# Performance work log

Hardware: AMD Instinct MI355X
Metric: run time of the kernel (lower is better)

## Reference

```python
import jax, jax.numpy as jnp
import numpy as np

B, S, D, H = 2, 2048, 1024, 16
DK = D // H

def setup_inputs() -> dict:
    key = jax.random.key(0)
    k1, k2, k3 = jax.random.split(key, 3)
    std = 2.0 / (D + 3 * D)
    x = jax.random.normal(k1, (B, S, D), dtype=jnp.float32)
    W_qkv = jax.random.normal(k2, (3 * D, D), dtype=jnp.float32) * std
    W_out = jax.random.normal(k3, (D, D), dtype=jnp.float32) * (2.0 / (2 * D))
    return {"x": x, "W_qkv": W_qkv, "W_out": W_out}

def reference(x, W_qkv, W_out):
    # fused QKV projection: [..., d_in] x [d_out, d_in] -> [..., d_out]
    proj = jnp.einsum('bsd,ed->bse', x, W_qkv)               # [B,S,3*H*DK]
    proj = proj.reshape(B, S, 3, H, DK)
    q = proj[:, :, 0].transpose(0, 2, 1, 3)                  # [B,H,S,DK]
    k = proj[:, :, 1].transpose(0, 2, 1, 3)
    v = proj[:, :, 2].transpose(0, 2, 1, 3)
    scores = jnp.einsum('bhnd,bhmd->bhnm', q, k) / jnp.sqrt(jnp.float32(DK))
    causal = jnp.tril(jnp.ones((S, S), dtype=bool))
    scores = jnp.where(causal, scores, -jnp.inf)
    attn = jax.nn.softmax(scores, axis=-1)
    out = jnp.einsum('bhnm,bhmd->bhnd', attn, v)             # [B,H,S,DK]
    out = out.transpose(0, 2, 1, 3).reshape(B, S, H * DK)
    return jnp.einsum('bsd,ed->bse', out, W_out)             # [B,S,D]
```

## Files before the change

kernel.cpp:

```cpp
#include <hip/hip_runtime.h>
#include <hip/hip_bf16.h>
#include <stdint.h>

typedef __attribute__((ext_vector_type(8))) __bf16 bf16x8;
typedef __attribute__((ext_vector_type(8))) short  short8;
typedef __attribute__((ext_vector_type(4))) float  f32x4;

#define MFMA16(a, b, c) __builtin_amdgcn_mfma_f32_16x16x32_bf16((a), (b), (c), 0, 0, 0)

__device__ __forceinline__ unsigned short f32_bf16(float f) {
  union { float f; unsigned u; } v; v.f = f;
  unsigned r = v.u + 0x7FFFu + ((v.u >> 16) & 1u);
  return (unsigned short)(r >> 16);
}

__device__ __forceinline__ void gload16(const unsigned short* g, unsigned short* l) {
  __builtin_amdgcn_global_load_lds(
      (const __attribute__((address_space(1))) unsigned int*)(g),
      (__attribute__((address_space(3))) unsigned int*)(l), 16, 0, 0);
}

__global__ void cvt3_kernel(const float* __restrict__ a, int na4,
                            const float* __restrict__ b, int nb4,
                            const float* __restrict__ c, int nc4,
                            unsigned short* __restrict__ oa,
                            unsigned short* __restrict__ ob,
                            unsigned short* __restrict__ oc) {
  int total = na4 + nb4 + nc4;
  for (int i = blockIdx.x * blockDim.x + threadIdx.x; i < total; i += gridDim.x * blockDim.x) {
    const float* src; unsigned short* dst; int j = i;
    if (j < na4) { src = a; dst = oa; }
    else if (j - na4 < nb4) { j -= na4; src = b; dst = ob; }
    else { j -= na4 + nb4; src = c; dst = oc; }
    float4 v = reinterpret_cast<const float4*>(src)[j];
    ushort4 o4;
    o4.x = f32_bf16(v.x); o4.y = f32_bf16(v.y);
    o4.z = f32_bf16(v.z); o4.w = f32_bf16(v.w);
    reinterpret_cast<ushort4*>(dst)[j] = o4;
  }
}

template <int MODE>
__global__ __launch_bounds__(256) void gemm_bt(const unsigned short* __restrict__ A,
                                               const unsigned short* __restrict__ Bm,
                                               void* __restrict__ Cout,
                                               int M, int N, int K) {
  __shared__ unsigned short As[128 * 32];
  __shared__ unsigned short Bs[128 * 32];
  __shared__ unsigned short Es[2 * 64 * 64];
  const int tid  = threadIdx.x;
  const int lane = tid & 63;
  const int wid  = tid >> 6;
  const int wr   = wid >> 1, wc = wid & 1;
  const int l16  = lane & 15, lh = lane >> 4;
  const int m0   = blockIdx.y * 128;
  const int n0   = blockIdx.x * 128;

  f32x4 acc[4][4];
#pragma unroll
  for (int mi = 0; mi < 4; ++mi)
#pragma unroll
    for (int ni = 0; ni < 4; ++ni) acc[mi][ni] = 0.f;

  const int c0 = tid, c1 = 256 + tid;
  const unsigned short* a0 = A + (size_t)(m0 + (c0 >> 2)) * K + (c0 & 3) * 8;
  const unsigned short* a1 = A + (size_t)(m0 + (c1 >> 2)) * K + (c1 & 3) * 8;
  const unsigned short* b0 = Bm + (size_t)(n0 + (c0 >> 2)) * K + (c0 & 3) * 8;
  const unsigned short* b1 = Bm + (size_t)(n0 + (c1 >> 2)) * K + (c1 & 3) * 8;
  const int d0 = wid * 64 * 8;
  const int d1 = (256 + wid * 64) * 8;

  for (int k0 = 0; k0 < K; k0 += 32) {
    __syncthreads();
    gload16(a0 + k0, As + d0);
    gload16(a1 + k0, As + d1);
    gload16(b0 + k0, Bs + d0);
    gload16(b1 + k0, Bs + d1);
    __syncthreads();
    bf16x8 af[4], bfr[4];
#pragma unroll
    for (int i = 0; i < 4; ++i) {
      af[i]  = *(const bf16x8*)(As + (wr * 64 + i * 16 + l16) * 32 + lh * 8);
      bfr[i] = *(const bf16x8*)(Bs + (wc * 64 + i * 16 + l16) * 32 + lh * 8);
    }
#pragma unroll
    for (int mi = 0; mi < 4; ++mi)
#pragma unroll
      for (int ni = 0; ni < 4; ++ni)
        acc[mi][ni] = MFMA16(af[mi], bfr[ni], acc[mi][ni]);
  }

  if (MODE == 0) {
    __syncthreads();
    unsigned short* Ep = (wid == 0) ? As : (wid == 1) ? Bs : Es + (wid - 2) * 4096;
    const int gn0 = n0 + wc * 64;
    const int cc  = gn0 >> 10;
    const int hh2 = (gn0 & 1023) >> 6;
    const int gm0 = m0 + wr * 64;
    const int bb2 = gm0 >> 11;
    const int ss0 = gm0 & 2047;
    const int bh2 = bb2 * 16 + hh2;
    unsigned short* qkv = (unsigned short*)Cout;

    if (cc < 2) {
      const float qsc = (cc == 0) ? 0.18033688f : 1.0f;
#pragma unroll
      for (int mi = 0; mi < 4; ++mi)
#pragma unroll
        for (int ni = 0; ni < 4; ++ni)
#pragma unroll
          for (int r = 0; r < 4; ++r) {
            int row = mi * 16 + lh * 4 + r;
            int col = (ni * 16 + l16) ^ (lh << 3);
            Ep[row * 64 + col] = f32_bf16(acc[mi][ni][r] * qsc);
          }
      unsigned short* qk = qkv + (((size_t)cc * 32 + bh2) * 2048 + ss0) * 64;
#pragma unroll
      for (int it = 0; it < 8; ++it) {
        int ci = it * 64 + lane;
        int row = ci >> 3, c = ci & 7;
        short8 vv = *(const short8*)(Ep + row * 64 + ((c ^ ((row >> 2) & 3)) * 8));
        *(short8*)(qk + (size_t)row * 64 + c * 8) = vv;
      }
    } else {
#pragma unroll
      for (int mi = 0; mi < 4; ++mi)
#pragma unroll
        for (int ni = 0; ni < 4; ++ni) {
          int dk = ni * 16 + l16;
          int ssl = mi * 16 + lh * 4;
          unsigned lo, hi;
          asm("v_cvt_pk_bf16_f32 %0, %1, %2" : "=v"(lo) : "v"(acc[mi][ni][0]), "v"(acc[mi][ni][1]));
          asm("v_cvt_pk_bf16_f32 %0, %1, %2" : "=v"(hi) : "v"(acc[mi][ni][2]), "v"(acc[mi][ni][3]));
          int off = dk * 64 + (ssl ^ ((dk & 7) << 3));
          *(uint2*)(Ep + off) = make_uint2(lo, hi);
        }
      unsigned short* vt = qkv + (size_t)8388608 + (size_t)bh2 * 64 * 2048 + ss0;
#pragma unroll
      for (int it = 0; it < 8; ++it) {
        int ci = it * 64 + lane;
        int dk = ci >> 3, c = ci & 7;
        short8 vv = *(const short8*)(Ep + dk * 64 + ((c ^ (dk & 7)) * 8));
        *(short8*)(vt + (size_t)dk * 2048 + c * 8) = vv;
      }
    }
  } else {
    float* C = (float*)Cout;
#pragma unroll
    for (int mi = 0; mi < 4; ++mi)
#pragma unroll
      for (int ni = 0; ni < 4; ++ni)
#pragma unroll
        for (int r = 0; r < 4; ++r) {
          int gm = m0 + wr * 64 + mi * 16 + lh * 4 + r;
          int gn = n0 + wc * 64 + ni * 16 + l16;
          C[(size_t)gm * N + gn] = acc[mi][ni][r];
        }
  }
}

__global__ __launch_bounds__(256) void attn_kernel(const unsigned short* __restrict__ Qg,
                                                   const unsigned short* __restrict__ Kg,
                                                   const unsigned short* __restrict__ Vtg,
                                                   unsigned short* __restrict__ Og) {
  __shared__ unsigned short Ks[2][64 * 64];
  __shared__ unsigned short Vs[2][64 * 64];
  __shared__ unsigned short Pl[4][16 * 64];

  const int tid  = threadIdx.x;
  const int lane = tid & 63;
  const int w    = tid >> 6;
  const int l16  = lane & 15, lh = lane >> 4;
  const int qt   = 31 - (blockIdx.x >> 5);
  const int bh   = blockIdx.x & 31;
  const int bb   = bh >> 4, hh = bh & 15;
  const int qb   = qt * 64;
  const int wqb  = qb + w * 16;

  const unsigned short* Qh = Qg + (size_t)bh * (2048 * 64);
  const unsigned short* Kh = Kg + (size_t)bh * (2048 * 64);
  const unsigned short* Vh = Vtg + (size_t)bh * (64 * 2048);

  bf16x8 qf[2];
#pragma unroll
  for (int h2 = 0; h2 < 2; ++h2)
    qf[h2] = *(const bf16x8*)(Qh + (size_t)(wqb + l16) * 64 + h2 * 32 + lh * 8);

  float mreg = 0.f;
  float ll   = 0.f;
  f32x4 o[4];
#pragma unroll
  for (int f = 0; f < 4; ++f) o[f] = 0.f;

  const int sA = tid, sB = tid + 256;
  const int rA = sA >> 3, hA = (sA & 7) ^ (rA & 7);
  const int rB = sB >> 3, hB = (sB & 7) ^ (rB & 7);
  const unsigned short* kSrcA = Kh + rA * 64 + hA * 8;
  const unsigned short* kSrcB = Kh + rB * 64 + hB * 8;
  const unsigned short* vSrcA = Vh + (size_t)rA * 2048 + hA * 8;
  const unsigned short* vSrcB = Vh + (size_t)rB * 2048 + hB * 8;
  const int ldsA = w * 64 * 8;
  const int ldsB = (256 + w * 64) * 8;

  const int sw = l16 & 7;
  const int ntiles = qt + 1;

  gload16(kSrcA, &Ks[0][ldsA]);
  gload16(kSrcB, &Ks[0][ldsB]);
  gload16(vSrcA, &Vs[0][ldsA]);
  gload16(vSrcB, &Vs[0][ldsB]);
  __syncthreads();

  for (int t = 0; t < ntiles; ++t) {
    const int kv0 = t * 64;
    const int cur = t & 1;
    if (t + 1 < ntiles) {
      const int nk = kv0 + 64;
      gload16(kSrcA + (size_t)nk * 64, &Ks[cur ^ 1][ldsA]);
      gload16(kSrcB + (size_t)nk * 64, &Ks[cur ^ 1][ldsB]);
      gload16(vSrcA + nk, &Vs[cur ^ 1][ldsA]);
      gload16(vSrcB + nk, &Vs[cur ^ 1][ldsB]);
    }

    if (kv0 <= wqb + 15) {
      const unsigned short* Kb = Ks[cur];
      const unsigned short* Vb = Vs[cur];

      f32x4 st[4];
#pragma unroll
      for (int tt = 0; tt < 4; ++tt) {
        const unsigned short* krow = Kb + (tt * 16 + l16) * 64;
        bf16x8 kf0 = *(const bf16x8*)(krow + ((lh ^ sw) * 8));
        bf16x8 kf1 = *(const bf16x8*)(krow + (((lh + 4) ^ sw) * 8));
        f32x4 a = {0.f, 0.f, 0.f, 0.f};
        a = MFMA16(kf0, qf[0], a);
        a = MFMA16(kf1, qf[1], a);
        st[tt] = a;
      }

      if (kv0 + 63 > wqb) {
        int qrow = wqb + l16;
#pragma unroll
        for (int tt = 0; tt < 4; ++tt) {
          int kvb = kv0 + tt * 16 + lh * 4;
#pragma unroll
          for (int r = 0; r < 4; ++r)
            if (kvb + r > qrow) st[tt][r] = -__builtin_inff();
        }
      }

      float pm = fmaxf(fmaxf(st[0][0], st[0][1]), fmaxf(st[0][2], st[0][3]));
#pragma unroll
      for (int tt = 1; tt < 4; ++tt)
        pm = fmaxf(pm, fmaxf(fmaxf(st[tt][0], st[tt][1]), fmaxf(st[tt][2], st[tt][3])));
      if (!__all(pm <= mreg + 8.f)) {
        float t0 = pm;
        t0 = fmaxf(t0, __shfl_xor(t0, 16));
        t0 = fmaxf(t0, __shfl_xor(t0, 32));
        float mn = fmaxf(mreg, t0);
        float er = exp2f(mreg - mn);
        mreg = mn;
        ll *= er;
#pragma unroll
        for (int r = 0; r < 4; ++r) {
          float e = __shfl(er, lh * 4 + r);
#pragma unroll
          for (int f = 0; f < 4; ++f) o[f][r] *= e;
        }
      }

      unsigned short* Pw = Pl[w];
      int rbase = l16 * 64;
      float ps = 0.f;
#pragma unroll
      for (int tt = 0; tt < 4; ++tt) {
        float p0 = exp2f(st[tt][0] - mreg);
        float p1 = exp2f(st[tt][1] - mreg);
        float p2 = exp2f(st[tt][2] - mreg);
        float p3 = exp2f(st[tt][3] - mreg);
        ps += (p0 + p1) + (p2 + p3);
        unsigned lo, hi;
        asm("v_cvt_pk_bf16_f32 %0, %1, %2" : "=v"(lo) : "v"(p0), "v"(p1));
        asm("v_cvt_pk_bf16_f32 %0, %1, %2" : "=v"(hi) : "v"(p2), "v"(p3));
        int c8 = tt * 2 + (lh >> 1);
        int off = rbase + ((c8 ^ sw) << 3) + (lh & 1) * 4;
        *(uint2*)(Pw + off) = make_uint2(lo, hi);
      }
      float rs = ps;
      rs += __shfl_xor(rs, 16);
      rs += __shfl_xor(rs, 32);
      ll += rs;

      bf16x8 pf0 = *(const bf16x8*)(Pw + rbase + ((lh ^ sw) * 8));
      bf16x8 pf1 = *(const bf16x8*)(Pw + rbase + (((lh + 4) ^ sw) * 8));
#pragma unroll
      for (int f = 0; f < 4; ++f) {
        const unsigned short* vrow = Vb + (f * 16 + l16) * 64;
        bf16x8 vf0 = *(const bf16x8*)(vrow + ((lh ^ sw) * 8));
        bf16x8 vf1 = *(const bf16x8*)(vrow + (((lh + 4) ^ sw) * 8));
        o[f] = MFMA16(pf0, vf0, o[f]);
        o[f] = MFMA16(pf1, vf1, o[f]);
      }
    }
    __syncthreads();
  }

  unsigned short* op = Og + (size_t)bb * 2048 * 1024 + (size_t)hh * 64;
#pragma unroll
  for (int r = 0; r < 4; ++r) {
    float linv = 1.f / __shfl(ll, lh * 4 + r);
    int row = wqb + lh * 4 + r;
#pragma unroll
    for (int f = 0; f < 4; ++f)
      op[(size_t)row * 1024 + f * 16 + l16] = f32_bf16(o[f][r] * linv);
  }
}

extern "C" void kernel_launch(void* const* d_in, const int* in_sizes, int n_in,
                              void* d_out, int out_size, void* d_ws, size_t ws_size,
                              hipStream_t stream) {
  const float* x    = (const float*)d_in[0];
  const float* Wqkv = (const float*)d_in[1];
  const float* Wout = (const float*)d_in[2];
  float* out = (float*)d_out;

  char* ws = (char*)d_ws;
  unsigned short* xb  = (unsigned short*)(ws);
  unsigned short* wqb = (unsigned short*)(ws + (size_t)8 * 1024 * 1024);
  unsigned short* wob = (unsigned short*)(ws + (size_t)14 * 1024 * 1024);
  unsigned short* qkv = (unsigned short*)(ws + (size_t)16 * 1024 * 1024);
  unsigned short* att = (unsigned short*)(ws + (size_t)40 * 1024 * 1024);

  cvt3_kernel<<<2048, 256, 0, stream>>>(x, 4194304 / 4, Wqkv, 3145728 / 4,
                                        Wout, 1048576 / 4, xb, wqb, wob);

  gemm_bt<0><<<dim3(24, 32), 256, 0, stream>>>(xb, wqb, (void*)qkv, 4096, 3072, 1024);

  const unsigned short* Qp  = qkv;
  const unsigned short* Kp  = qkv + 4194304;
  const unsigned short* Vtp = qkv + 8388608;
  attn_kernel<<<1024, 256, 0, stream>>>(Qp, Kp, Vtp, att);

  gemm_bt<1><<<dim3(8, 32), 256, 0, stream>>>(att, wob, (void*)out, 4096, 1024, 1024);
}
```

Measured before the change: 126.3 us.

## Stage output GEMM epilogue through LDS and rebalance causal attention scheduling

```diff
diff --git a/kernel.cpp b/kernel.cpp
--- a/kernel.cpp
+++ b/kernel.cpp
@@ -45,9 +45,9 @@
                                                const unsigned short* __restrict__ Bm,
                                                void* __restrict__ Cout,
                                                int M, int N, int K) {
-  __shared__ unsigned short As[128 * 32];
-  __shared__ unsigned short Bs[128 * 32];
-  __shared__ unsigned short Es[2 * 64 * 64];
+  extern __shared__ unsigned short SM[];
+  unsigned short* As = SM;
+  unsigned short* Bs = SM + 4096;
   const int tid  = threadIdx.x;
   const int lane = tid & 63;
   const int wid  = tid >> 6;
@@ -90,9 +90,10 @@
         acc[mi][ni] = MFMA16(af[mi], bfr[ni], acc[mi][ni]);
   }
 
+  __syncthreads();
+  unsigned short* Ep = SM + wid * 4096;
+
   if (MODE == 0) {
-    __syncthreads();
-    unsigned short* Ep = (wid == 0) ? As : (wid == 1) ? Bs : Es + (wid - 2) * 4096;
     const int gn0 = n0 + wc * 64;
     const int cc  = gn0 >> 10;
     const int hh2 = (gn0 & 1023) >> 6;
@@ -146,16 +147,31 @@
     }
   } else {
     float* C = (float*)Cout;
-#pragma unroll
-    for (int mi = 0; mi < 4; ++mi)
-#pragma unroll
-      for (int ni = 0; ni < 4; ++ni)
-#pragma unroll
-        for (int r = 0; r < 4; ++r) {
-          int gm = m0 + wr * 64 + mi * 16 + lh * 4 + r;
-          int gn = n0 + wc * 64 + ni * 16 + l16;
-          C[(size_t)gm * N + gn] = acc[mi][ni][r];
+    float* Ef = (float*)Ep;
+    const int gm0 = m0 + wr * 64;
+    const int gn0 = n0 + wc * 64;
+#pragma unroll
+    for (int p = 0; p < 2; ++p) {
+#pragma unroll
+      for (int mi = 0; mi < 4; ++mi)
+#pragma unroll
+        for (int q = 0; q < 2; ++q) {
+          int ni = 2 * p + q;
+#pragma unroll
+          for (int r = 0; r < 4; ++r) {
+            int row = mi * 16 + lh * 4 + r;
+            int col = (q * 16 + l16) ^ ((row & 7) << 2);
+            Ef[row * 32 + col] = acc[mi][ni][r];
+          }
         }
+#pragma unroll
+      for (int it = 0; it < 8; ++it) {
+        int ci = it * 64 + lane;
+        int row = ci >> 3, c4 = ci & 7;
+        float4 vv = *(const float4*)(Ef + row * 32 + ((c4 * 4) ^ ((row & 7) << 2)));
+        *(float4*)(&C[(size_t)(gm0 + row) * N + gn0 + p * 32 + c4 * 4]) = vv;
+      }
+    }
   }
 }
 
@@ -171,7 +187,9 @@
   const int lane = tid & 63;
   const int w    = tid >> 6;
   const int l16  = lane & 15, lh = lane >> 4;
-  const int qt   = 31 - (blockIdx.x >> 5);
+  const int j    = blockIdx.x >> 5;
+  const int ring = j >> 3, k = j & 7;
+  const int qt   = (ring == 0) ? 31 - k : (ring == 1) ? k : (ring == 2) ? 23 - k : 8 + k;
   const int bh   = blockIdx.x & 31;
   const int bb   = bh >> 4, hh = bh & 15;
   const int qb   = qt * 64;
@@ -222,9 +240,10 @@
       gload16(vSrcB + nk, &Vs[cur ^ 1][ldsB]);
     }
 
-    if (kv0 <= wqb + 15) {
+    {
       const unsigned short* Kb = Ks[cur];
       const unsigned short* Vb = Vs[cur];
+      __builtin_amdgcn_s_setprio(1);
 
       f32x4 st[4];
 #pragma unroll
@@ -301,6 +320,7 @@
         o[f] = MFMA16(pf0, vf0, o[f]);
         o[f] = MFMA16(pf1, vf1, o[f]);
       }
+      __builtin_amdgcn_s_setprio(0);
     }
     __syncthreads();
   }
@@ -334,12 +354,12 @@
   cvt3_kernel<<<2048, 256, 0, stream>>>(x, 4194304 / 4, Wqkv, 3145728 / 4,
                                         Wout, 1048576 / 4, xb, wqb, wob);
 
-  gemm_bt<0><<<dim3(24, 32), 256, 0, stream>>>(xb, wqb, (void*)qkv, 4096, 3072, 1024);
+  gemm_bt<0><<<dim3(24, 32), 256, 32768, stream>>>(xb, wqb, (void*)qkv, 4096, 3072, 1024);
 
   const unsigned short* Qp  = qkv;
   const unsigned short* Kp  = qkv + 4194304;
   const unsigned short* Vtp = qkv + 8388608;
   attn_kernel<<<1024, 256, 0, stream>>>(Qp, Kp, Vtp, att);
 
-  gemm_bt<1><<<dim3(8, 32), 256, 0, stream>>>(att, wob, (void*)out, 4096, 1024, 1024);
-}
+  gemm_bt<1><<<dim3(8, 32), 256, 32768, stream>>>(att, wob, (void*)out, 4096, 1024, 1024);
+}
```

Result: no change. 125.9 us (-0.3%).
